# Kernel tuning notes

Measured on AMD Instinct MI355X. Metric: run time of the kernel, lower is better.

Reference implementation:

```python
import jax, jax.numpy as jnp
import numpy as np
from jax import lax

ALPHA, OMEGA, EPSILON, THETA, W_MASK = 2.1, 14.0, 1.0, 0.5, 10.0


def setup_inputs() -> dict:
    key = jax.random.key(0)
    k1, k2 = jax.random.split(key)
    shape = (64, 68, 128, 128)
    pred = jax.random.uniform(k1, shape, dtype=jnp.float32)
    landmark = jax.random.uniform(k2, shape, dtype=jnp.float32)
    return {"pred": pred, "landmark": landmark}


def _weight_mask(landmark):
    # replicate cv2: round(heatmap*255), 3x3 rect dilation (max filter), threshold at 0.2*h
    hm = jnp.round(landmark * 255.0)
    dil = lax.reduce_window(hm, -jnp.inf, lax.max,
                            window_dimensions=(1, 1, 3, 3),
                            window_strides=(1, 1, 1, 1),
                            padding='SAME')
    h = landmark.shape[2]  # h == w in the original thresholding
    return (dil >= h * 0.2).astype(landmark.dtype)


def _awing(pred, landmark):
    diff = jnp.abs(pred - landmark)
    asl = ALPHA - landmark                      # alpha - y, elementwise exponent
    tde = THETA / EPSILON
    T1 = tde ** asl
    T2 = tde ** (asl - 1.0)
    A = OMEGA / (1.0 + T1) * asl * T2 / EPSILON
    C = THETA * A - OMEGA * jnp.log1p(T1)
    return jnp.where(diff < THETA,
                     OMEGA * jnp.log1p((diff / EPSILON) ** asl),
                     A * diff - C)


def reference(pred, landmark):
    M = _weight_mask(landmark)
    loss = _awing(pred, landmark) * (W_MASK * M + 1.0)
    return jnp.mean(loss)
```

## Files before the change

kernel.cpp:

```cpp
#include <hip/hip_runtime.h>

constexpr int H = 128, W = 128;
constexpr int IMG = H * W;
constexpr int STRIP = 32;
constexpr int STRIPS = H / STRIP;

__device__ __forceinline__ float max3f(float a, float b, float c) {
    return fmaxf(fmaxf(a, b), c);
}
__device__ __forceinline__ float exp2_hw(float x) { return __builtin_amdgcn_exp2f(x); }
__device__ __forceinline__ float log2_hw(float x) { return __builtin_amdgcn_logf(x); }
__device__ __forceinline__ float rcp_hw(float x)  { return __builtin_amdgcn_rcpf(x); }

__global__ __launch_bounds__(256, 8) void awing_partial(
    const float* __restrict__ pred,
    const float* __restrict__ lmk,
    float* __restrict__ part)
{
    __shared__ __align__(16) float s[(STRIP + 2) * W];
    __shared__ float wsum[4];

    const int tid  = threadIdx.x;
    const int img  = blockIdx.x >> 2;
    const int st   = blockIdx.x & 3;
    const int row0 = st * STRIP;
    const float* li = lmk  + (size_t)img * IMG;
    const float* pi = pred + (size_t)img * IMG;

    for (int s4 = tid; s4 < (STRIP + 2) * (W / 4); s4 += 256) {
        int lr = s4 >> 5;
        int c4 = s4 & 31;
        int gr = row0 - 1 + lr;
        gr = min(max(gr, 0), H - 1);
        ((float4*)s)[s4] = ((const float4*)li)[gr * (W / 4) + c4];
    }
    __syncthreads();

    const bool leftEdge  = (tid & 31) == 0;
    const bool rightEdge = (tid & 31) == 31;

    float acc = 0.0f;
#pragma unroll
    for (int it = 0; it < 4; ++it) {
        int e  = it * 1024 + tid * 4;
        int rl = e >> 7;
        int c  = e & 127;

        float4 p4 = ((const float4*)pi)[(row0 + rl) * 32 + (c >> 2)];

        int b0 = rl * W + c;
        float4 a4 = *(const float4*)&s[b0];
        float4 b4 = *(const float4*)&s[b0 + W];
        float4 d4 = *(const float4*)&s[b0 + 2 * W];

        float v0 = max3f(a4.x, b4.x, d4.x);
        float v1 = max3f(a4.y, b4.y, d4.y);
        float v2 = max3f(a4.z, b4.z, d4.z);
        float v3 = max3f(a4.w, b4.w, d4.w);
        float vL = __shfl_up(v3, 1, 64);
        float vR = __shfl_down(v0, 1, 64);
        vL = leftEdge  ? v0 : vL;
        vR = rightEdge ? v3 : vR;

        float mm[4] = { max3f(vL, v0, v1), max3f(v0, v1, v2),
                        max3f(v1, v2, v3), max3f(v2, v3, vR) };
        float yy[4] = { b4.x, b4.y, b4.z, b4.w };
        float pp[4] = { p4.x, p4.y, p4.z, p4.w };

#pragma unroll
        for (int j = 0; j < 4; ++j) {
            float y    = yy[j];
            float d    = fabsf(pp[j] - y);
            float asl  = 2.1f - y;
            bool  lo   = d < 0.5f;
            float L    = log2_hw(d);
            float beta = lo ? asl * L : -asl;
            float E    = exp2_hw(beta);
            float S    = 1.0f + E;
            float G    = log2_hw(S);
            float A    = 28.0f * asl * E * rcp_hw(S);
            float Asel = lo ? 0.0f : A;
            float lossv = fmaf(Asel, d - 0.5f, 9.704060527839234f * G);
            float wgt  = (mm[j] * 255.0f >= 25.5f) ? 11.0f : 1.0f;
            acc = fmaf(lossv, wgt, acc);
        }
    }

#pragma unroll
    for (int off = 32; off > 0; off >>= 1) acc += __shfl_down(acc, off, 64);
    if ((tid & 63) == 0) wsum[tid >> 6] = acc;
    __syncthreads();
    if (tid == 0) part[blockIdx.x] = (wsum[0] + wsum[1]) + (wsum[2] + wsum[3]);
}

__global__ void final_reduce(const float* __restrict__ part, int n,
                             float* __restrict__ out, double inv_total)
{
    __shared__ double sd[4];
    int tid = threadIdx.x;
    double a = 0.0;
    for (int i = tid; i < n; i += 256) a += (double)part[i];
#pragma unroll
    for (int off = 32; off > 0; off >>= 1) a += __shfl_down(a, off, 64);
    if ((tid & 63) == 0) sd[tid >> 6] = a;
    __syncthreads();
    if (tid == 0) out[0] = (float)((sd[0] + sd[1] + sd[2] + sd[3]) * inv_total);
}

extern "C" void kernel_launch(void* const* d_in, const int* in_sizes, int n_in,
                              void* d_out, int out_size, void* d_ws, size_t ws_size,
                              hipStream_t stream)
{
    const float* pred = (const float*)d_in[0];
    const float* lmk  = (const float*)d_in[1];
    float* part = (float*)d_ws;
    int total   = in_sizes[0];
    int nimg    = total / IMG;
    int nblocks = nimg * STRIPS;

    awing_partial<<<nblocks, 256, 0, stream>>>(pred, lmk, part);
    final_reduce<<<1, 256, 0, stream>>>(part, nblocks, (float*)d_out,
                                        1.0 / (double)total);
}
```

Baseline: 542.4 us.

## Stream strip rows through a register rolling window instead of shared memory

Each 32-lane group now processes one 32-row strip on its own, walking down the rows and keeping a rotating window of four landmark rows in registers for the 3x3 max filter. This replaces the shared-memory staging and the block-wide barrier, and the next row's pred values are prefetched one step ahead. Eight strips are packed per 256-thread block, so the grid has fewer blocks. In exchange, each thread does more serial work and there are fewer threads in flight to hide load latency.

```diff
diff --git a/kernel.cpp b/kernel.cpp
--- a/kernel.cpp
+++ b/kernel.cpp
@@ -4,6 +4,7 @@
 constexpr int IMG = H * W;
 constexpr int STRIP = 32;
 constexpr int STRIPS = H / STRIP;
+constexpr int UNITS_PER_BLOCK = 8;
 
 __device__ __forceinline__ float max3f(float a, float b, float c) {
     return fmaxf(fmaxf(a, b), c);
@@ -17,74 +18,71 @@
     const float* __restrict__ lmk,
     float* __restrict__ part)
 {
-    __shared__ __align__(16) float s[(STRIP + 2) * W];
     __shared__ float wsum[4];
 
     const int tid  = threadIdx.x;
-    const int img  = blockIdx.x >> 2;
-    const int st   = blockIdx.x & 3;
+    const int lane = tid & 31;
+    const int unit = blockIdx.x * UNITS_PER_BLOCK + (tid >> 5);
+    const int img  = unit >> 2;
+    const int st   = unit & 3;
     const int row0 = st * STRIP;
-    const float* li = lmk  + (size_t)img * IMG;
-    const float* pi = pred + (size_t)img * IMG;
+    const float4* l4 = (const float4*)(lmk  + (size_t)img * IMG);
+    const float4* p4 = (const float4*)(pred + (size_t)img * IMG);
 
-    for (int s4 = tid; s4 < (STRIP + 2) * (W / 4); s4 += 256) {
-        int lr = s4 >> 5;
-        int c4 = s4 & 31;
-        int gr = row0 - 1 + lr;
-        gr = min(max(gr, 0), H - 1);
-        ((float4*)s)[s4] = ((const float4*)li)[gr * (W / 4) + c4];
-    }
-    __syncthreads();
+    const bool le = (lane == 0), re = (lane == 31);
 
-    const bool leftEdge  = (tid & 31) == 0;
-    const bool rightEdge = (tid & 31) == 31;
+    float4 A = l4[max(row0 - 1, 0) * 32 + lane];
+    float4 B = l4[row0 * 32 + lane];
+    float4 C = l4[(row0 + 1) * 32 + lane];
+    float4 D;
+    float4 P = p4[row0 * 32 + lane];
 
     float acc = 0.0f;
-#pragma unroll
-    for (int it = 0; it < 4; ++it) {
-        int e  = it * 1024 + tid * 4;
-        int rl = e >> 7;
-        int c  = e & 127;
 
-        float4 p4 = ((const float4*)pi)[(row0 + rl) * 32 + (c >> 2)];
+#define ROW_STEP(A_, B_, C_, D_, r_)                                         \
+    {                                                                        \
+        D_ = l4[min((r_) + 2, H - 1) * 32 + lane];      \
+        float4 Pn = p4[min((r_) + 1, H - 1) * 32 + lane];        \
+        float v0 = max3f(A_.x, B_.x, C_.x);                                  \
+        float v1 = max3f(A_.y, B_.y, C_.y);                                  \
+        float v2 = max3f(A_.z, B_.z, C_.z);                                  \
+        float v3 = max3f(A_.w, B_.w, C_.w);                                  \
+        float vL = __shfl_up(v3, 1, 32);                                     \
+        float vR = __shfl_down(v0, 1, 32);                                   \
+        vL = le ? v0 : vL;        \
+        vR = re ? v3 : vR;                                                   \
+        float mm[4] = { max3f(vL, v0, v1), max3f(v0, v1, v2),                \
+                        max3f(v1, v2, v3), max3f(v2, v3, vR) };              \
+        float yy[4] = { B_.x, B_.y, B_.z, B_.w };                            \
+        float pp[4] = { P.x, P.y, P.z, P.w };                                \
+        _Pragma("unroll")                                                    \
+        for (int j = 0; j < 4; ++j) {                                        \
+            float y    = yy[j];                                              \
+            float d    = fabsf(pp[j] - y);                                   \
+            float asl  = 2.1f - y;                        \
+            bool  lo   = d < 0.5f;                                           \
+            float L    = log2_hw(d);             \
+            float beta = lo ? asl * L : -asl;                                \
+            float E    = exp2_hw(beta);                                      \
+            float S    = 1.0f + E;                                           \
+            float G    = log2_hw(S);                                         \
+            float Aw   = 28.0f * asl * E * rcp_hw(S);         \
+            float Asel = lo ? 0.0f : Aw;                                     \
+            float lossv = fmaf(Asel, d - 0.5f, 9.704060527839234f * G);      \
+               \
+            float wgt  = (mm[j] * 255.0f >= 25.5f) ? 11.0f : 1.0f;           \
+            acc = fmaf(lossv, wgt, acc);                                     \
+        }                                                                    \
+        P = Pn;                                                              \
+    }
 
-        int b0 = rl * W + c;
-        float4 a4 = *(const float4*)&s[b0];
-        float4 b4 = *(const float4*)&s[b0 + W];
-        float4 d4 = *(const float4*)&s[b0 + 2 * W];
-
-        float v0 = max3f(a4.x, b4.x, d4.x);
-        float v1 = max3f(a4.y, b4.y, d4.y);
-        float v2 = max3f(a4.z, b4.z, d4.z);
-        float v3 = max3f(a4.w, b4.w, d4.w);
-        float vL = __shfl_up(v3, 1, 64);
-        float vR = __shfl_down(v0, 1, 64);
-        vL = leftEdge  ? v0 : vL;
-        vR = rightEdge ? v3 : vR;
-
-        float mm[4] = { max3f(vL, v0, v1), max3f(v0, v1, v2),
-                        max3f(v1, v2, v3), max3f(v2, v3, vR) };
-        float yy[4] = { b4.x, b4.y, b4.z, b4.w };
-        float pp[4] = { p4.x, p4.y, p4.z, p4.w };
-
-#pragma unroll
-        for (int j = 0; j < 4; ++j) {
-            float y    = yy[j];
-            float d    = fabsf(pp[j] - y);
-            float asl  = 2.1f - y;
-            bool  lo   = d < 0.5f;
-            float L    = log2_hw(d);
-            float beta = lo ? asl * L : -asl;
-            float E    = exp2_hw(beta);
-            float S    = 1.0f + E;
-            float G    = log2_hw(S);
-            float A    = 28.0f * asl * E * rcp_hw(S);
-            float Asel = lo ? 0.0f : A;
-            float lossv = fmaf(Asel, d - 0.5f, 9.704060527839234f * G);
-            float wgt  = (mm[j] * 255.0f >= 25.5f) ? 11.0f : 1.0f;
-            acc = fmaf(lossv, wgt, acc);
-        }
+    for (int r = row0; r < row0 + STRIP; r += 4) {
+        ROW_STEP(A, B, C, D, r)
+        ROW_STEP(B, C, D, A, r + 1)
+        ROW_STEP(C, D, A, B, r + 2)
+        ROW_STEP(D, A, B, C, r + 3)
     }
+#undef ROW_STEP
 
 #pragma unroll
     for (int off = 32; off > 0; off >>= 1) acc += __shfl_down(acc, off, 64);
@@ -116,7 +114,8 @@
     float* part = (float*)d_ws;
     int total   = in_sizes[0];
     int nimg    = total / IMG;
-    int nblocks = nimg * STRIPS;
+    int nunits  = nimg * STRIPS;
+    int nblocks = nunits / UNITS_PER_BLOCK;
 
     awing_partial<<<nblocks, 256, 0, stream>>>(pred, lmk, part);
     final_reduce<<<1, 256, 0, stream>>>(part, nblocks, (float*)d_out,
```

Measured after the change: 541.1 us. No clear change (-0.2%).

## Replace LDS halo staging with per-half-wave register sliding window over rows

Applied to the files above, without the earlier changes.

Each 32-lane group now owns a 32-row strip and walks down it, keeping a rolling 5-row window of landmark rows and a 3-row window of pred rows in registers. This removes the shared-memory tile, its fill loop and the block barrier, and prefetches the next rows while computing the current one. In exchange it raises register pressure and the load pattern changes from one wide coalesced tile fill to per-row float4 loads per half-wave. Block count drops by a factor of eight, and the grid assumes the number of units divides evenly by eight.

```diff
diff --git a/kernel.cpp b/kernel.cpp
--- a/kernel.cpp
+++ b/kernel.cpp
@@ -4,6 +4,7 @@
 constexpr int IMG = H * W;
 constexpr int STRIP = 32;
 constexpr int STRIPS = H / STRIP;
+constexpr int UNITS_PER_BLOCK = 8;
 
 __device__ __forceinline__ float max3f(float a, float b, float c) {
     return fmaxf(fmaxf(a, b), c);
@@ -17,55 +18,53 @@
     const float* __restrict__ lmk,
     float* __restrict__ part)
 {
-    __shared__ __align__(16) float s[(STRIP + 2) * W];
     __shared__ float wsum[4];
 
     const int tid  = threadIdx.x;
-    const int img  = blockIdx.x >> 2;
-    const int st   = blockIdx.x & 3;
+    const int lane = tid & 31;
+    const int unit = blockIdx.x * UNITS_PER_BLOCK + (tid >> 5);
+    const int img  = unit >> 2;
+    const int st   = unit & 3;
     const int row0 = st * STRIP;
-    const float* li = lmk  + (size_t)img * IMG;
-    const float* pi = pred + (size_t)img * IMG;
+    const float4* l4 = (const float4*)(lmk  + (size_t)img * IMG) + lane;
+    const float4* p4 = (const float4*)(pred + (size_t)img * IMG) + lane;
 
-    for (int s4 = tid; s4 < (STRIP + 2) * (W / 4); s4 += 256) {
-        int lr = s4 >> 5;
-        int c4 = s4 & 31;
-        int gr = row0 - 1 + lr;
-        gr = min(max(gr, 0), H - 1);
-        ((float4*)s)[s4] = ((const float4*)li)[gr * (W / 4) + c4];
-    }
-    __syncthreads();
+    const bool le = (lane == 0), re = (lane == 31);
 
-    const bool leftEdge  = (tid & 31) == 0;
-    const bool rightEdge = (tid & 31) == 31;
+    float4 L[5], P[3];
+    L[0] = l4[max(row0 - 1, 0) * 32];
+    L[1] = l4[(row0 + 0) * 32];
+    L[2] = l4[(row0 + 1) * 32];
+    L[3] = l4[(row0 + 2) * 32];
+    P[0] = p4[(row0 + 0) * 32];
+    P[1] = p4[(row0 + 1) * 32];
 
     float acc = 0.0f;
+
 #pragma unroll
-    for (int it = 0; it < 4; ++it) {
-        int e  = it * 1024 + tid * 4;
-        int rl = e >> 7;
-        int c  = e & 127;
+    for (int k = 0; k < STRIP; ++k) {
+        const int r = row0 + k;
+        L[(k + 4) % 5] = l4[min(r + 3, H - 1) * 32];
+        P[(k + 2) % 3] = p4[min(r + 2, H - 1) * 32];
 
-        float4 p4 = ((const float4*)pi)[(row0 + rl) * 32 + (c >> 2)];
+        const float4 Ar = L[k % 5];
+        const float4 Br = L[(k + 1) % 5];
+        const float4 Cr = L[(k + 2) % 5];
+        const float4 Pr = P[k % 3];
 
-        int b0 = rl * W + c;
-        float4 a4 = *(const float4*)&s[b0];
-        float4 b4 = *(const float4*)&s[b0 + W];
-        float4 d4 = *(const float4*)&s[b0 + 2 * W];
+        float v0 = max3f(Ar.x, Br.x, Cr.x);
+        float v1 = max3f(Ar.y, Br.y, Cr.y);
+        float v2 = max3f(Ar.z, Br.z, Cr.z);
+        float v3 = max3f(Ar.w, Br.w, Cr.w);
+        float vL = __shfl_up(v3, 1, 32);
+        float vR = __shfl_down(v0, 1, 32);
+        vL = le ? v0 : vL;
+        vR = re ? v3 : vR;
 
-        float v0 = max3f(a4.x, b4.x, d4.x);
-        float v1 = max3f(a4.y, b4.y, d4.y);
-        float v2 = max3f(a4.z, b4.z, d4.z);
-        float v3 = max3f(a4.w, b4.w, d4.w);
-        float vL = __shfl_up(v3, 1, 64);
-        float vR = __shfl_down(v0, 1, 64);
-        vL = leftEdge  ? v0 : vL;
-        vR = rightEdge ? v3 : vR;
-
-        float mm[4] = { max3f(vL, v0, v1), max3f(v0, v1, v2),
-                        max3f(v1, v2, v3), max3f(v2, v3, vR) };
-        float yy[4] = { b4.x, b4.y, b4.z, b4.w };
-        float pp[4] = { p4.x, p4.y, p4.z, p4.w };
+        const float mm[4] = { max3f(vL, v0, v1), max3f(v0, v1, v2),
+                              max3f(v1, v2, v3), max3f(v2, v3, vR) };
+        const float yy[4] = { Br.x, Br.y, Br.z, Br.w };
+        const float pp[4] = { Pr.x, Pr.y, Pr.z, Pr.w };
 
 #pragma unroll
         for (int j = 0; j < 4; ++j) {
@@ -73,13 +72,13 @@
             float d    = fabsf(pp[j] - y);
             float asl  = 2.1f - y;
             bool  lo   = d < 0.5f;
-            float L    = log2_hw(d);
-            float beta = lo ? asl * L : -asl;
+            float Lg   = log2_hw(d);
+            float beta = lo ? asl * Lg : -asl;
             float E    = exp2_hw(beta);
             float S    = 1.0f + E;
             float G    = log2_hw(S);
-            float A    = 28.0f * asl * E * rcp_hw(S);
-            float Asel = lo ? 0.0f : A;
+            float Aw   = 28.0f * asl * E * rcp_hw(S);
+            float Asel = lo ? 0.0f : Aw;
             float lossv = fmaf(Asel, d - 0.5f, 9.704060527839234f * G);
             float wgt  = (mm[j] * 255.0f >= 25.5f) ? 11.0f : 1.0f;
             acc = fmaf(lossv, wgt, acc);
@@ -116,7 +115,8 @@
     float* part = (float*)d_ws;
     int total   = in_sizes[0];
     int nimg    = total / IMG;
-    int nblocks = nimg * STRIPS;
+    int nunits  = nimg * STRIPS;
+    int nblocks = nunits / UNITS_PER_BLOCK;
 
     awing_partial<<<nblocks, 256, 0, stream>>>(pred, lmk, part);
     final_reduce<<<1, 256, 0, stream>>>(part, nblocks, (float*)d_out,
```

After: 542.8 us. About the same (+0.1%).
